# Optimization experiments

Hardware: AMD Instinct MI355X
Metric: run time of the kernel (lower is better)

The kernel has to match this reference:

```python
import jax, jax.numpy as jnp
import numpy as np

B, N, D, M = 16, 8192, 512, 1024


def setup_inputs() -> dict:
    key = jax.random.key(0)
    k1, k2 = jax.random.split(key)
    x = jax.random.normal(k1, (B, N, D), dtype=jnp.float32)
    mem = jax.random.normal(k2, (1, D, M), dtype=jnp.float32)  # learned memory bank
    return {"x": x, "mem": mem}


def reference(x, mem):
    # forward_mem: memory-slot cross-attention
    # x: [B, N, D]; mem: [1, D, M] (broadcast over batch)
    d = x.shape[-1]
    m = mem[0]  # [D, M]
    # logits[b, m, n] = sum_d mem[d, m] * x[b, n, d] / sqrt(D)  -> [B, M, N]
    logits = jnp.einsum('dm,bnd->bmn', m, x) / jnp.sqrt(jnp.asarray(d, x.dtype))
    # softmax over the memory-slot axis (dim=1 in torch == axis 1 here)
    attn = jax.nn.softmax(logits, axis=1)  # [B, M, N]
    # x_new[b, n, d] = sum_m mem[d, m] * attn[b, m, n]
    out = jnp.einsum('dm,bmn->bnd', m, attn)  # [B, N, D]
    return out
```

## Files before the change

kernel.cpp:

```cpp
#include <hip/hip_runtime.h>

#define B_ 16
#define N_ 8192
#define D_ 512
#define M_ 1024
#define BT 64
#define XPAD 520
#define PPAD 72
#define SCALE 0.04419417382415922f

typedef __attribute__((ext_vector_type(8))) short short8;
typedef __attribute__((ext_vector_type(4))) short short4v;
typedef __attribute__((ext_vector_type(4))) float f32x4;

__device__ __forceinline__ unsigned short f2bf(float f) {
  unsigned int u = __float_as_uint(f);
  u += 0x7FFFu + ((u >> 16) & 1u);
  return (unsigned short)(u >> 16);
}
__device__ __forceinline__ float bf2f(unsigned short h) {
  return __uint_as_float(((unsigned int)h) << 16);
}

#define MFMA(a, b, c) __builtin_amdgcn_mfma_f32_16x16x32_bf16((a), (b), (c), 0, 0, 0)

__global__ void prep_mem_kernel(const float* __restrict__ mem,
                                unsigned short* __restrict__ memTb,
                                unsigned short* __restrict__ memb) {
  int idx = blockIdx.x * 256 + threadIdx.x;
  float v = mem[idx];
  unsigned short b = f2bf(v);
  int d = idx >> 10;
  int m = idx & (M_ - 1);
  memb[idx] = b;
  memTb[m * D_ + d] = b;
}

__global__ __launch_bounds__(256, 2) void fused_kernel(
    const float* __restrict__ x, const unsigned short* __restrict__ memTb,
    const unsigned short* __restrict__ memb, float* __restrict__ out) {
  __shared__ unsigned short sX[BT * XPAD];
  __shared__ unsigned short sPa[BT * PPAD];
  __shared__ float psums[4][BT];
  __shared__ float sInvS[BT];

  const int tid = threadIdx.x;
  const int w = tid >> 6;
  const int lane = tid & 63;
  const int r = lane & 15;
  const int g = lane >> 4;
  const long t0 = (long)blockIdx.x * BT;

  {
    const int row = tid >> 2;
    const int cb = (tid & 3) * 8;
    const float* xp = x + (t0 + row) * (long)D_;
    unsigned short* dst = &sX[row * XPAD];
#pragma unroll
    for (int j = 0; j < 16; j++) {
      const int c = cb + j * 32;
      f32x4 v0 = *(const f32x4*)(xp + c);
      f32x4 v1 = *(const f32x4*)(xp + c + 4);
      short8 o;
      o[0] = (short)f2bf(v0[0] * SCALE);
      o[1] = (short)f2bf(v0[1] * SCALE);
      o[2] = (short)f2bf(v0[2] * SCALE);
      o[3] = (short)f2bf(v0[3] * SCALE);
      o[4] = (short)f2bf(v1[0] * SCALE);
      o[5] = (short)f2bf(v1[1] * SCALE);
      o[6] = (short)f2bf(v1[2] * SCALE);
      o[7] = (short)f2bf(v1[3] * SCALE);
      *(short8*)(dst + c) = o;
    }
  }
  __syncthreads();

  f32x4 oacc[4][8];
#pragma unroll
  for (int tb = 0; tb < 4; tb++)
#pragma unroll
    for (int d0 = 0; d0 < 8; d0++) oacc[tb][d0] = (f32x4){0.f, 0.f, 0.f, 0.f};

  float fsum[4] = {0.f, 0.f, 0.f, 0.f};
  f32x4 acc[4];

  auto gemm1 = [&](int cbase) {
#pragma unroll
    for (int tb = 0; tb < 4; tb++) acc[tb] = (f32x4){0.f, 0.f, 0.f, 0.f};
    const unsigned short* ap = memTb + (size_t)(cbase + w * 16 + r) * D_ + g * 8;
#pragma unroll 4
    for (int k0 = 0; k0 < 16; k0++) {
      short8 a = *(const short8*)(ap + k0 * 32);
      short8 xv0 = *(const short8*)(&sX[(0 * 16 + r) * XPAD + k0 * 32 + g * 8]);
      short8 xv1 = *(const short8*)(&sX[(1 * 16 + r) * XPAD + k0 * 32 + g * 8]);
      short8 xv2 = *(const short8*)(&sX[(2 * 16 + r) * XPAD + k0 * 32 + g * 8]);
      short8 xv3 = *(const short8*)(&sX[(3 * 16 + r) * XPAD + k0 * 32 + g * 8]);
      acc[0] = MFMA(a, xv0, acc[0]);
      acc[1] = MFMA(a, xv1, acc[1]);
      acc[2] = MFMA(a, xv2, acc[2]);
      acc[3] = MFMA(a, xv3, acc[3]);
    }
  };

  auto pgen = [&]() {
#pragma unroll
    for (int tb = 0; tb < 4; tb++) {
      short4v o;
      float s = 0.f;
#pragma unroll
      for (int i = 0; i < 4; i++) {
        float p = __expf(acc[tb][i]);
        unsigned short pb = f2bf(p);
        o[i] = (short)pb;
        s += bf2f(pb);
      }
      fsum[tb] += s;
      *(short4v*)(&sPa[(tb * 16 + r) * PPAD + w * 16 + g * 4]) = o;
    }
  };

  gemm1(0);
  pgen();

#pragma unroll 1
  for (int c = 0; c < 16; c++) {
    __syncthreads();
    {
      const unsigned short* bbase =
          memb + (size_t)(w * 128 + r) * M_ + c * 64 + g * 8;
#pragma unroll
      for (int kk = 0; kk < 2; kk++) {
        short8 pa0 = *(const short8*)(&sPa[(0 * 16 + r) * PPAD + kk * 32 + g * 8]);
        short8 pa1 = *(const short8*)(&sPa[(1 * 16 + r) * PPAD + kk * 32 + g * 8]);
        short8 pa2 = *(const short8*)(&sPa[(2 * 16 + r) * PPAD + kk * 32 + g * 8]);
        short8 pa3 = *(const short8*)(&sPa[(3 * 16 + r) * PPAD + kk * 32 + g * 8]);
#pragma unroll
        for (int d0 = 0; d0 < 8; d0++) {
          short8 mb = *(const short8*)(bbase + (size_t)d0 * 16 * M_ + kk * 32);
          oacc[0][d0] = MFMA(pa0, mb, oacc[0][d0]);
          oacc[1][d0] = MFMA(pa1, mb, oacc[1][d0]);
          oacc[2][d0] = MFMA(pa2, mb, oacc[2][d0]);
          oacc[3][d0] = MFMA(pa3, mb, oacc[3][d0]);
        }
      }
    }
    if (c < 15) gemm1((c + 1) * 64);
    __syncthreads();
    if (c < 15) pgen();
  }

#pragma unroll
  for (int tb = 0; tb < 4; tb++) {
    float s = fsum[tb];
    s += __shfl_xor(s, 16);
    s += __shfl_xor(s, 32);
    if (g == 0) psums[w][tb * 16 + r] = s;
  }
  __syncthreads();
  if (tid < BT)
    sInvS[tid] = 1.0f / (psums[0][tid] + psums[1][tid] + psums[2][tid] + psums[3][tid]);
  __syncthreads();

  {
    const int dq = w * 128;
#pragma unroll
    for (int tb = 0; tb < 4; tb++) {
#pragma unroll
      for (int i = 0; i < 4; i++) {
        const int tok = tb * 16 + g * 4 + i;
        const float inv = sInvS[tok];
        float* op = out + (t0 + tok) * (long)D_ + dq + r;
#pragma unroll
        for (int d0 = 0; d0 < 8; d0++) op[d0 * 16] = oacc[tb][d0][i] * inv;
      }
    }
  }
}

extern "C" void kernel_launch(void* const* d_in, const int* in_sizes, int n_in,
                              void* d_out, int out_size, void* d_ws, size_t ws_size,
                              hipStream_t stream) {
  const float* x = (const float*)d_in[0];
  const float* mem = (const float*)d_in[1];
  float* out = (float*)d_out;
  unsigned short* memTb = (unsigned short*)d_ws;
  unsigned short* memb = memTb + (size_t)D_ * M_;

  hipLaunchKernelGGL(prep_mem_kernel, dim3((D_ * M_) / 256), dim3(256), 0, stream,
                     mem, memTb, memb);
  hipLaunchKernelGGL(fused_kernel, dim3((B_ * N_) / BT), dim3(256), 0, stream,
                     x, memTb, memb, out);
}
```

Before: 557.1 us.

## Double block to eight waves, split GEMM work, and XOR-swizzle LDS tiles

The fused block grows from 4 to 8 waves. In the logits GEMM each wave now covers 16 memory slots by 32 tokens. In the output GEMM each wave owns 64 output columns instead of 128, so per-wave accumulators are halved. Padded shared-memory rows are replaced by an XOR swizzle on 16-byte chunks to avoid bank conflicts without extra LDS. The aim is more latency hiding and more concurrent MFMA issue per CU. The risks are the tighter register budget implied by the new launch bounds, which may cause spills, and the larger unpadded 64 KB X tile, which limits how many blocks fit per CU.

```diff
diff --git a/kernel.cpp b/kernel.cpp
--- a/kernel.cpp
+++ b/kernel.cpp
@@ -5,8 +5,6 @@
 #define D_ 512
 #define M_ 1024
 #define BT 64
-#define XPAD 520
-#define PPAD 72
 #define SCALE 0.04419417382415922f
 
 typedef __attribute__((ext_vector_type(8))) short short8;
@@ -36,11 +34,32 @@
   memTb[m * D_ + d] = b;
 }
 
-__global__ __launch_bounds__(256, 2) void fused_kernel(
+__device__ __forceinline__ const short8* sx_rd(const unsigned short* sX, int row, int colE) {
+  int byte = (row << 10) + (colE << 1);
+  byte ^= (row & 7) << 4;
+  return (const short8*)((const char*)sX + byte);
+}
+__device__ __forceinline__ short8* sx_wr(unsigned short* sX, int row, int colE) {
+  int byte = (row << 10) + (colE << 1);
+  byte ^= (row & 7) << 4;
+  return (short8*)((char*)sX + byte);
+}
+__device__ __forceinline__ const short8* sp_rd(const unsigned short* sPa, int row, int colE) {
+  int byte = (row << 7) + (colE << 1);
+  byte ^= (row & 7) << 4;
+  return (const short8*)((const char*)sPa + byte);
+}
+__device__ __forceinline__ short4v* sp_wr(unsigned short* sPa, int row, int colE) {
+  int byte = (row << 7) + (colE << 1);
+  byte ^= (row & 7) << 4;
+  return (short4v*)((char*)sPa + byte);
+}
+
+__global__ __launch_bounds__(512, 4) void fused_kernel(
     const float* __restrict__ x, const unsigned short* __restrict__ memTb,
     const unsigned short* __restrict__ memb, float* __restrict__ out) {
-  __shared__ unsigned short sX[BT * XPAD];
-  __shared__ unsigned short sPa[BT * PPAD];
+  __shared__ unsigned short sX[BT * D_];
+  __shared__ unsigned short sPa[BT * 64];
   __shared__ float psums[4][BT];
   __shared__ float sInvS[BT];
 
@@ -49,18 +68,19 @@
   const int lane = tid & 63;
   const int r = lane & 15;
   const int g = lane >> 4;
+  const int mslot = w & 3;
+  const int tokbase = (w >> 2) * 32;
   const long t0 = (long)blockIdx.x * BT;
 
   {
-    const int row = tid >> 2;
-    const int cb = (tid & 3) * 8;
+    const int row = tid >> 3;
+    const int cslot = tid & 7;
     const float* xp = x + (t0 + row) * (long)D_;
-    unsigned short* dst = &sX[row * XPAD];
-#pragma unroll
-    for (int j = 0; j < 16; j++) {
-      const int c = cb + j * 32;
-      f32x4 v0 = *(const f32x4*)(xp + c);
-      f32x4 v1 = *(const f32x4*)(xp + c + 4);
+#pragma unroll
+    for (int j = 0; j < 8; j++) {
+      const int cE = cslot * 8 + j * 64;
+      f32x4 v0 = *(const f32x4*)(xp + cE);
+      f32x4 v1 = *(const f32x4*)(xp + cE + 4);
       short8 o;
       o[0] = (short)f2bf(v0[0] * SCALE);
       o[1] = (short)f2bf(v0[1] * SCALE);
@@ -70,41 +90,37 @@
       o[5] = (short)f2bf(v1[1] * SCALE);
       o[6] = (short)f2bf(v1[2] * SCALE);
       o[7] = (short)f2bf(v1[3] * SCALE);
-      *(short8*)(dst + c) = o;
+      *sx_wr(sX, row, cE) = o;
     }
   }
   __syncthreads();
 
-  f32x4 oacc[4][8];
+  f32x4 oacc[4][4];
 #pragma unroll
   for (int tb = 0; tb < 4; tb++)
 #pragma unroll
-    for (int d0 = 0; d0 < 8; d0++) oacc[tb][d0] = (f32x4){0.f, 0.f, 0.f, 0.f};
-
-  float fsum[4] = {0.f, 0.f, 0.f, 0.f};
-  f32x4 acc[4];
+    for (int d0 = 0; d0 < 4; d0++) oacc[tb][d0] = (f32x4){0.f, 0.f, 0.f, 0.f};
+
+  float fsum[2] = {0.f, 0.f};
+  f32x4 acc[2];
 
   auto gemm1 = [&](int cbase) {
 #pragma unroll
-    for (int tb = 0; tb < 4; tb++) acc[tb] = (f32x4){0.f, 0.f, 0.f, 0.f};
-    const unsigned short* ap = memTb + (size_t)(cbase + w * 16 + r) * D_ + g * 8;
+    for (int tb = 0; tb < 2; tb++) acc[tb] = (f32x4){0.f, 0.f, 0.f, 0.f};
+    const unsigned short* ap = memTb + (size_t)(cbase + mslot * 16 + r) * D_ + g * 8;
 #pragma unroll 4
     for (int k0 = 0; k0 < 16; k0++) {
       short8 a = *(const short8*)(ap + k0 * 32);
-      short8 xv0 = *(const short8*)(&sX[(0 * 16 + r) * XPAD + k0 * 32 + g * 8]);
-      short8 xv1 = *(const short8*)(&sX[(1 * 16 + r) * XPAD + k0 * 32 + g * 8]);
-      short8 xv2 = *(const short8*)(&sX[(2 * 16 + r) * XPAD + k0 * 32 + g * 8]);
-      short8 xv3 = *(const short8*)(&sX[(3 * 16 + r) * XPAD + k0 * 32 + g * 8]);
+      short8 xv0 = *sx_rd(sX, tokbase + r, k0 * 32 + g * 8);
+      short8 xv1 = *sx_rd(sX, tokbase + 16 + r, k0 * 32 + g * 8);
       acc[0] = MFMA(a, xv0, acc[0]);
       acc[1] = MFMA(a, xv1, acc[1]);
-      acc[2] = MFMA(a, xv2, acc[2]);
-      acc[3] = MFMA(a, xv3, acc[3]);
     }
   };
 
   auto pgen = [&]() {
 #pragma unroll
-    for (int tb = 0; tb < 4; tb++) {
+    for (int tb = 0; tb < 2; tb++) {
       short4v o;
       float s = 0.f;
 #pragma unroll
@@ -115,7 +131,7 @@
         s += bf2f(pb);
       }
       fsum[tb] += s;
-      *(short4v*)(&sPa[(tb * 16 + r) * PPAD + w * 16 + g * 4]) = o;
+      *sp_wr(sPa, tokbase + tb * 16 + r, mslot * 16 + g * 4) = o;
     }
   };
 
@@ -127,15 +143,15 @@
     __syncthreads();
     {
       const unsigned short* bbase =
-          memb + (size_t)(w * 128 + r) * M_ + c * 64 + g * 8;
+          memb + (size_t)(w * 64 + r) * M_ + c * 64 + g * 8;
 #pragma unroll
       for (int kk = 0; kk < 2; kk++) {
-        short8 pa0 = *(const short8*)(&sPa[(0 * 16 + r) * PPAD + kk * 32 + g * 8]);
-        short8 pa1 = *(const short8*)(&sPa[(1 * 16 + r) * PPAD + kk * 32 + g * 8]);
-        short8 pa2 = *(const short8*)(&sPa[(2 * 16 + r) * PPAD + kk * 32 + g * 8]);
-        short8 pa3 = *(const short8*)(&sPa[(3 * 16 + r) * PPAD + kk * 32 + g * 8]);
-#pragma unroll
-        for (int d0 = 0; d0 < 8; d0++) {
+        short8 pa0 = *sp_rd(sPa, 0 * 16 + r, kk * 32 + g * 8);
+        short8 pa1 = *sp_rd(sPa, 1 * 16 + r, kk * 32 + g * 8);
+        short8 pa2 = *sp_rd(sPa, 2 * 16 + r, kk * 32 + g * 8);
+        short8 pa3 = *sp_rd(sPa, 3 * 16 + r, kk * 32 + g * 8);
+#pragma unroll
+        for (int d0 = 0; d0 < 4; d0++) {
           short8 mb = *(const short8*)(bbase + (size_t)d0 * 16 * M_ + kk * 32);
           oacc[0][d0] = MFMA(pa0, mb, oacc[0][d0]);
           oacc[1][d0] = MFMA(pa1, mb, oacc[1][d0]);
@@ -150,11 +166,11 @@
   }
 
 #pragma unroll
-  for (int tb = 0; tb < 4; tb++) {
+  for (int tb = 0; tb < 2; tb++) {
     float s = fsum[tb];
     s += __shfl_xor(s, 16);
     s += __shfl_xor(s, 32);
-    if (g == 0) psums[w][tb * 16 + r] = s;
+    if (g == 0) psums[mslot][tokbase + tb * 16 + r] = s;
   }
   __syncthreads();
   if (tid < BT)
@@ -162,7 +178,7 @@
   __syncthreads();
 
   {
-    const int dq = w * 128;
+    const int dq = w * 64;
 #pragma unroll
     for (int tb = 0; tb < 4; tb++) {
 #pragma unroll
@@ -171,7 +187,7 @@
         const float inv = sInvS[tok];
         float* op = out + (t0 + tok) * (long)D_ + dq + r;
 #pragma unroll
-        for (int d0 = 0; d0 < 8; d0++) op[d0 * 16] = oacc[tb][d0][i] * inv;
+        for (int d0 = 0; d0 < 4; d0++) op[d0 * 16] = oacc[tb][d0][i] * inv;
       }
     }
   }
@@ -188,6 +204,6 @@
 
   hipLaunchKernelGGL(prep_mem_kernel, dim3((D_ * M_) / 256), dim3(256), 0, stream,
                      mem, memTb, memb);
-  hipLaunchKernelGGL(fused_kernel, dim3((B_ * N_) / BT), dim3(256), 0, stream,
+  hipLaunchKernelGGL(fused_kernel, dim3((B_ * N_) / BT), dim3(512), 0, stream,
                      x, memTb, memb, out);
 }
```

Result: slower. 756.4 us (+35.8%).

## Switch to 32x32x16 MFMA with fragment-ordered memory and swizzled LDS

Applied to the files above, without the earlier changes.

Replaces the 16x16x32 bf16 MFMA tiles with 32x32x16 tiles and processes 128 memory slots per chunk (8 chunks instead of 16). The prep kernel now stores both memory copies pre-arranged in per-lane fragment order, with the scale folded into the first copy, so global loads are contiguous per lane. Padded LDS rows are replaced by XOR-swizzled layouts. The next chunk's logits GEMM is interleaved into the output GEMM loop, and the softmax normalisation is merged into the final loop iteration. This aims for fewer, larger MFMA issues, coalesced operand loads and better overlap, at the cost of larger accumulator register use under the 2-blocks-per-CU bound.

```diff
diff --git a/kernel.cpp b/kernel.cpp
--- a/kernel.cpp
+++ b/kernel.cpp
@@ -5,13 +5,12 @@
 #define D_ 512
 #define M_ 1024
 #define BT 64
-#define XPAD 520
-#define PPAD 72
 #define SCALE 0.04419417382415922f
 
 typedef __attribute__((ext_vector_type(8))) short short8;
 typedef __attribute__((ext_vector_type(4))) short short4v;
 typedef __attribute__((ext_vector_type(4))) float f32x4;
+typedef __attribute__((ext_vector_type(16))) float f32x16;
 
 __device__ __forceinline__ unsigned short f2bf(float f) {
   unsigned int u = __float_as_uint(f);
@@ -22,100 +21,118 @@
   return __uint_as_float(((unsigned int)h) << 16);
 }
 
-#define MFMA(a, b, c) __builtin_amdgcn_mfma_f32_16x16x32_bf16((a), (b), (c), 0, 0, 0)
+#define MFMA32(a, b, c) __builtin_amdgcn_mfma_f32_32x32x16_bf16((a), (b), (c), 0, 0, 0)
 
 __global__ void prep_mem_kernel(const float* __restrict__ mem,
-                                unsigned short* __restrict__ memTb,
-                                unsigned short* __restrict__ memb) {
-  int idx = blockIdx.x * 256 + threadIdx.x;
-  float v = mem[idx];
-  unsigned short b = f2bf(v);
-  int d = idx >> 10;
-  int m = idx & (M_ - 1);
-  memb[idx] = b;
-  memTb[m * D_ + d] = b;
+                                unsigned short* __restrict__ memTbF,
+                                unsigned short* __restrict__ memDF) {
+  int t = blockIdx.x * 256 + threadIdx.x;
+  int j = t & 7, l = (t >> 3) & 63, blk = t >> 9;
+  {
+    int kk = blk & 31, MT = blk >> 5;
+    int m = MT * 32 + (l & 31);
+    int d = kk * 16 + ((l >> 5) << 3) + j;
+    memTbF[t] = f2bf(mem[d * M_ + m] * SCALE);
+  }
+  {
+    int kg = blk & 63, DT = blk >> 6;
+    int d = DT * 32 + (l & 31);
+    int m = kg * 16 + ((l >> 5) << 3) + j;
+    memDF[t] = f2bf(mem[d * M_ + m]);
+  }
 }
 
 __global__ __launch_bounds__(256, 2) void fused_kernel(
-    const float* __restrict__ x, const unsigned short* __restrict__ memTb,
-    const unsigned short* __restrict__ memb, float* __restrict__ out) {
-  __shared__ unsigned short sX[BT * XPAD];
-  __shared__ unsigned short sPa[BT * PPAD];
-  __shared__ float psums[4][BT];
-  __shared__ float sInvS[BT];
+    const float* __restrict__ x, const unsigned short* __restrict__ memTbF,
+    const unsigned short* __restrict__ memDF, float* __restrict__ out) {
+  __shared__ unsigned short sX[32768];
+  __shared__ unsigned short sPa[8192];
+  float* psums = (float*)sX;
+  float* sInv = ((float*)sX) + 256;
 
   const int tid = threadIdx.x;
   const int w = tid >> 6;
   const int lane = tid & 63;
-  const int r = lane & 15;
-  const int g = lane >> 4;
+  const int c31 = lane & 31;
+  const int l5 = lane >> 5;
+  const int e7 = lane & 7;
+  const int t15 = c31 & 15;
   const long t0 = (long)blockIdx.x * BT;
 
   {
-    const int row = tid >> 2;
-    const int cb = (tid & 3) * 8;
-    const float* xp = x + (t0 + row) * (long)D_;
-    unsigned short* dst = &sX[row * XPAD];
+    const int row = tid >> 2, cg = tid & 3;
+    const int r7 = row & 7;
+    const float* xp = x + (t0 + row) * (long)D_ + cg * 128;
+    char* sxb = (char*)sX + (row << 10);
 #pragma unroll
     for (int j = 0; j < 16; j++) {
-      const int c = cb + j * 32;
-      f32x4 v0 = *(const f32x4*)(xp + c);
-      f32x4 v1 = *(const f32x4*)(xp + c + 4);
+      f32x4 v0 = *(const f32x4*)(xp + j * 8);
+      f32x4 v1 = *(const f32x4*)(xp + j * 8 + 4);
       short8 o;
-      o[0] = (short)f2bf(v0[0] * SCALE);
-      o[1] = (short)f2bf(v0[1] * SCALE);
-      o[2] = (short)f2bf(v0[2] * SCALE);
-      o[3] = (short)f2bf(v0[3] * SCALE);
-      o[4] = (short)f2bf(v1[0] * SCALE);
-      o[5] = (short)f2bf(v1[1] * SCALE);
-      o[6] = (short)f2bf(v1[2] * SCALE);
-      o[7] = (short)f2bf(v1[3] * SCALE);
-      *(short8*)(dst + c) = o;
+      o[0] = (short)f2bf(v0[0]);
+      o[1] = (short)f2bf(v0[1]);
+      o[2] = (short)f2bf(v0[2]);
+      o[3] = (short)f2bf(v0[3]);
+      o[4] = (short)f2bf(v1[0]);
+      o[5] = (short)f2bf(v1[1]);
+      o[6] = (short)f2bf(v1[2]);
+      o[7] = (short)f2bf(v1[3]);
+      int s = (cg << 4) + j;
+      *(short8*)(sxb + ((s ^ r7) << 4)) = o;
     }
   }
   __syncthreads();
 
-  f32x4 oacc[4][8];
-#pragma unroll
-  for (int tb = 0; tb < 4; tb++)
-#pragma unroll
-    for (int d0 = 0; d0 < 8; d0++) oacc[tb][d0] = (f32x4){0.f, 0.f, 0.f, 0.f};
-
-  float fsum[4] = {0.f, 0.f, 0.f, 0.f};
-  f32x4 acc[4];
-
-  auto gemm1 = [&](int cbase) {
-#pragma unroll
-    for (int tb = 0; tb < 4; tb++) acc[tb] = (f32x4){0.f, 0.f, 0.f, 0.f};
-    const unsigned short* ap = memTb + (size_t)(cbase + w * 16 + r) * D_ + g * 8;
-#pragma unroll 4
-    for (int k0 = 0; k0 < 16; k0++) {
-      short8 a = *(const short8*)(ap + k0 * 32);
-      short8 xv0 = *(const short8*)(&sX[(0 * 16 + r) * XPAD + k0 * 32 + g * 8]);
-      short8 xv1 = *(const short8*)(&sX[(1 * 16 + r) * XPAD + k0 * 32 + g * 8]);
-      short8 xv2 = *(const short8*)(&sX[(2 * 16 + r) * XPAD + k0 * 32 + g * 8]);
-      short8 xv3 = *(const short8*)(&sX[(3 * 16 + r) * XPAD + k0 * 32 + g * 8]);
-      acc[0] = MFMA(a, xv0, acc[0]);
-      acc[1] = MFMA(a, xv1, acc[1]);
-      acc[2] = MFMA(a, xv2, acc[2]);
-      acc[3] = MFMA(a, xv3, acc[3]);
+  f32x16 oacc[2][4];
+#pragma unroll
+  for (int tt = 0; tt < 2; tt++)
+#pragma unroll
+    for (int d0 = 0; d0 < 4; d0++) oacc[tt][d0] = (f32x16)0.0f;
+  f32x16 sacc[2];
+  float fsum[2] = {0.f, 0.f};
+
+  char* const bx0 = (char*)sX + (c31 << 10);
+  char* const bx1 = (char*)sX + ((32 + c31) << 10);
+  char* const bp0 = (char*)sPa + (c31 << 8);
+  char* const bp1 = (char*)sPa + ((32 + c31) << 8);
+
+  auto gemm1 = [&](int ch) {
+    sacc[0] = (f32x16)0.0f;
+    sacc[1] = (f32x16)0.0f;
+    const short8* ga = (const short8*)memTbF + (size_t)((ch * 4 + w) * 32) * 64 + lane;
+#pragma unroll
+    for (int kk = 0; kk < 32; kk++) {
+      short8 a = ga[kk * 64];
+      int sw = (((kk << 1) | l5) ^ e7) << 4;
+      short8 x0 = *(const short8*)(bx0 + sw);
+      short8 x1 = *(const short8*)(bx1 + sw);
+      sacc[0] = MFMA32(a, x0, sacc[0]);
+      sacc[1] = MFMA32(a, x1, sacc[1]);
     }
   };
 
   auto pgen = [&]() {
 #pragma unroll
-    for (int tb = 0; tb < 4; tb++) {
-      short4v o;
+    for (int tt = 0; tt < 2; tt++) {
+      int tok = tt * 32 + c31;
+      char* base = (char*)sPa + (tok << 8);
       float s = 0.f;
-#pragma unroll
-      for (int i = 0; i < 4; i++) {
-        float p = __expf(acc[tb][i]);
-        unsigned short pb = f2bf(p);
-        o[i] = (short)pb;
-        s += bf2f(pb);
-      }
-      fsum[tb] += s;
-      *(short4v*)(&sPa[(tb * 16 + r) * PPAD + w * 16 + g * 4]) = o;
+      unsigned short pb[16];
+#pragma unroll
+      for (int q = 0; q < 16; q++) {
+        float p = __expf(sacc[tt][q]);
+        unsigned short b = f2bf(p);
+        pb[q] = b;
+        s += bf2f(b);
+      }
+      fsum[tt] += s;
+#pragma unroll
+      for (int q = 0; q < 4; q++) {
+        short4v o = {(short)pb[q * 4], (short)pb[q * 4 + 1],
+                     (short)pb[q * 4 + 2], (short)pb[q * 4 + 3]};
+        int sl = ((w << 2) | q) ^ t15;
+        *(short4v*)(base + (sl << 4) + (l5 << 3)) = o;
+      }
     }
   };
 
@@ -123,56 +140,75 @@
   pgen();
 
 #pragma unroll 1
-  for (int c = 0; c < 16; c++) {
+  for (int c = 0; c < 8; c++) {
     __syncthreads();
+    if (c == 7 && tid < BT) {
+      float s = psums[tid] + psums[64 + tid] + psums[128 + tid] + psums[192 + tid];
+      sInv[tid] = 1.0f / s;
+    }
     {
-      const unsigned short* bbase =
-          memb + (size_t)(w * 128 + r) * M_ + c * 64 + g * 8;
-#pragma unroll
-      for (int kk = 0; kk < 2; kk++) {
-        short8 pa0 = *(const short8*)(&sPa[(0 * 16 + r) * PPAD + kk * 32 + g * 8]);
-        short8 pa1 = *(const short8*)(&sPa[(1 * 16 + r) * PPAD + kk * 32 + g * 8]);
-        short8 pa2 = *(const short8*)(&sPa[(2 * 16 + r) * PPAD + kk * 32 + g * 8]);
-        short8 pa3 = *(const short8*)(&sPa[(3 * 16 + r) * PPAD + kk * 32 + g * 8]);
-#pragma unroll
-        for (int d0 = 0; d0 < 8; d0++) {
-          short8 mb = *(const short8*)(bbase + (size_t)d0 * 16 * M_ + kk * 32);
-          oacc[0][d0] = MFMA(pa0, mb, oacc[0][d0]);
-          oacc[1][d0] = MFMA(pa1, mb, oacc[1][d0]);
-          oacc[2][d0] = MFMA(pa2, mb, oacc[2][d0]);
-          oacc[3][d0] = MFMA(pa3, mb, oacc[3][d0]);
+      const short8* gb = (const short8*)memDF + ((size_t)(w * 4) * 64 + c * 8) * 64 + lane;
+      const bool doG1 = (c < 7);
+      const short8* ga = (const short8*)memTbF +
+                         (size_t)((((c + 1) & 7) * 4 + w) * 32) * 64 + lane;
+      if (doG1) {
+        sacc[0] = (f32x16)0.0f;
+        sacc[1] = (f32x16)0.0f;
+      }
+#pragma unroll
+      for (int k0 = 0; k0 < 8; k0++) {
+        int sp = ((((k0 << 1) | l5) ^ t15) << 4);
+        short8 p0 = *(const short8*)(bp0 + sp);
+        short8 p1 = *(const short8*)(bp1 + sp);
+        short8 b0 = gb[(0 * 64 + k0) * 64];
+        short8 b1 = gb[(1 * 64 + k0) * 64];
+        short8 b2 = gb[(2 * 64 + k0) * 64];
+        short8 b3 = gb[(3 * 64 + k0) * 64];
+        oacc[0][0] = MFMA32(p0, b0, oacc[0][0]);
+        oacc[1][0] = MFMA32(p1, b0, oacc[1][0]);
+        oacc[0][1] = MFMA32(p0, b1, oacc[0][1]);
+        oacc[1][1] = MFMA32(p1, b1, oacc[1][1]);
+        oacc[0][2] = MFMA32(p0, b2, oacc[0][2]);
+        oacc[1][2] = MFMA32(p1, b2, oacc[1][2]);
+        oacc[0][3] = MFMA32(p0, b3, oacc[0][3]);
+        oacc[1][3] = MFMA32(p1, b3, oacc[1][3]);
+        if (doG1) {
+#pragma unroll
+          for (int kq = 0; kq < 4; kq++) {
+            int kk = k0 * 4 + kq;
+            short8 a = ga[kk * 64];
+            int sw = (((kk << 1) | l5) ^ e7) << 4;
+            short8 x0 = *(const short8*)(bx0 + sw);
+            short8 x1 = *(const short8*)(bx1 + sw);
+            sacc[0] = MFMA32(a, x0, sacc[0]);
+            sacc[1] = MFMA32(a, x1, sacc[1]);
+          }
         }
       }
     }
-    if (c < 15) gemm1((c + 1) * 64);
     __syncthreads();
-    if (c < 15) pgen();
-  }
-
-#pragma unroll
-  for (int tb = 0; tb < 4; tb++) {
-    float s = fsum[tb];
-    s += __shfl_xor(s, 16);
-    s += __shfl_xor(s, 32);
-    if (g == 0) psums[w][tb * 16 + r] = s;
-  }
-  __syncthreads();
-  if (tid < BT)
-    sInvS[tid] = 1.0f / (psums[0][tid] + psums[1][tid] + psums[2][tid] + psums[3][tid]);
-  __syncthreads();
-
-  {
-    const int dq = w * 128;
-#pragma unroll
-    for (int tb = 0; tb < 4; tb++) {
-#pragma unroll
-      for (int i = 0; i < 4; i++) {
-        const int tok = tb * 16 + g * 4 + i;
-        const float inv = sInvS[tok];
-        float* op = out + (t0 + tok) * (long)D_ + dq + r;
-#pragma unroll
-        for (int d0 = 0; d0 < 8; d0++) op[d0 * 16] = oacc[tb][d0][i] * inv;
-      }
+    if (c < 7) {
+      pgen();
+      if (c == 6) {
+        float s0 = fsum[0] + __shfl_xor(fsum[0], 32);
+        float s1 = fsum[1] + __shfl_xor(fsum[1], 32);
+        if (lane < 32) {
+          psums[w * 64 + lane] = s0;
+          psums[w * 64 + 32 + lane] = s1;
+        }
+      }
+    }
+  }
+
+#pragma unroll
+  for (int tt = 0; tt < 2; tt++) {
+#pragma unroll
+    for (int q = 0; q < 16; q++) {
+      int tok = tt * 32 + (q & 3) + ((q >> 2) << 3) + (l5 << 2);
+      float inv = sInv[tok];
+      float* op = out + (t0 + tok) * (long)D_ + w * 128 + c31;
+#pragma unroll
+      for (int d0 = 0; d0 < 4; d0++) op[d0 * 32] = oacc[tt][d0][q] * inv;
     }
   }
 }
@@ -183,11 +219,11 @@
   const float* x = (const float*)d_in[0];
   const float* mem = (const float*)d_in[1];
   float* out = (float*)d_out;
-  unsigned short* memTb = (unsigned short*)d_ws;
-  unsigned short* memb = memTb + (size_t)D_ * M_;
+  unsigned short* memTbF = (unsigned short*)d_ws;
+  unsigned short* memDF = memTbF + (size_t)D_ * M_;
 
   hipLaunchKernelGGL(prep_mem_kernel, dim3((D_ * M_) / 256), dim3(256), 0, stream,
-                     mem, memTb, memb);
+                     mem, memTbF, memDF);
   hipLaunchKernelGGL(fused_kernel, dim3((B_ * N_) / BT), dim3(256), 0, stream,
-                     x, memTb, memb, out);
-}
+                     x, memTbF, memDF, out);
+}
```

Result: faster. 452.2 us (-18.8%).
